# Kernel optimization log

Measured on AMD Instinct MI355X. Metric: run time of the kernel, lower is better.

Reference implementation:

```python
import jax, jax.numpy as jnp
import numpy as np
import math

B, C, N, M, K, TEMB, H = 16, 64, 4096, 257, 128, 256, 128
PI = math.pi

def _inv_sp(y):
    return math.log(math.expm1(y))

def setup_inputs():
    key = jax.random.key(0)
    ks = jax.random.split(key, 8)
    x_feat = jax.random.normal(ks[0], (B, C, N), jnp.float32)
    z = (jax.random.uniform(ks[1], (B, N), jnp.float32) * 2.0 - 1.0) * PI
    temb = jax.random.normal(ks[2], (B, TEMB), jnp.float32)
    kappa_pos_raw = jnp.full((K,), _inv_sp(0.3), jnp.float32)
    gabor_c = jnp.linspace(-1.0, 1.0, M).astype(jnp.float32)
    gabor_omega_raw = jnp.full((M,), _inv_sp(0.25), jnp.float32)
    wr = (jax.random.normal(ks[3], (C, M)) * 0.02).astype(jnp.float32)
    wi = (jax.random.normal(ks[4], (C, M)) * 0.02).astype(jnp.float32)
    bias = jnp.zeros((1, C, 1), jnp.float32)
    tproj_w = (jax.random.normal(ks[5], (C, TEMB)) * 0.02).astype(jnp.float32)
    tproj_b = jnp.zeros((C,), jnp.float32)
    mlp_w1 = (jax.random.normal(ks[6], (H, TEMB)) * 0.02).astype(jnp.float32)
    mlp_b1 = jnp.zeros((H,), jnp.float32)
    mlp_w2 = (jax.random.normal(ks[7], (1, H)) * 0.02).astype(jnp.float32)
    mlp_b2 = jnp.zeros((1,), jnp.float32)
    # tau0 = 0.15-quantile of |kappa_init| (matches ProgressiveFreqGate init)
    kpos0 = np.cumsum(np.log1p(np.exp(_inv_sp(0.3))) * np.ones(K, np.float64))
    kfull = np.concatenate([-kpos0[::-1], [0.0], kpos0])
    tau0 = jnp.float32(np.quantile(np.abs(kfull), 0.15))
    tau1_raw = jnp.float32(_inv_sp(0.5))
    alpha_raw = jnp.float32(_inv_sp(8.0))
    gate_low_raw = jnp.float32(4.0)
    gate_mid_raw = jnp.float32(-2.1972246)
    gate_high_raw = jnp.float32(-2.1972246)
    return dict(x_feat=x_feat, z=z, temb=temb, kappa_pos_raw=kappa_pos_raw,
                gabor_c=gabor_c, gabor_omega_raw=gabor_omega_raw, wr=wr, wi=wi,
                bias=bias, tproj_w=tproj_w, tproj_b=tproj_b, mlp_w1=mlp_w1,
                mlp_b1=mlp_b1, mlp_w2=mlp_w2, mlp_b2=mlp_b2, tau0=tau0,
                tau1_raw=tau1_raw, alpha_raw=alpha_raw, gate_low_raw=gate_low_raw,
                gate_mid_raw=gate_mid_raw, gate_high_raw=gate_high_raw)

def reference(x_feat, z, temb, kappa_pos_raw, gabor_c, gabor_omega_raw, wr, wi, bias,
              tproj_w, tproj_b, mlp_w1, mlp_b1, mlp_w2, mlp_b2,
              tau0, tau1_raw, alpha_raw, gate_low_raw, gate_mid_raw, gate_high_raw):
    sp = jax.nn.softplus
    # non-uniform learned frequencies: kappa = [-kpos[::-1], 0, kpos]
    kpos = jnp.cumsum(sp(kappa_pos_raw))                      # (K,)
    kappa = jnp.concatenate([-kpos[::-1], jnp.zeros((1,), kpos.dtype), kpos])  # (M,)
    k_abs = jax.lax.stop_gradient(jnp.abs(kappa))
    # band mask: quantile thresholds (detached), learnable low/mid/high gates
    th1 = jnp.quantile(k_abs, 0.4)
    th2 = jnp.quantile(k_abs, 0.8)
    g_low = jax.nn.sigmoid(gate_low_raw)
    g_mid = jax.nn.sigmoid(gate_mid_raw)
    g_high = jax.nn.sigmoid(gate_high_raw)
    band = jnp.where(k_abs <= th1, g_low, jnp.where(k_abs <= th2, g_mid, g_high))  # (M,)
    # progressive time-frequency gate: g = sigmoid(alpha*(tau(t) - |kappa|))
    hid = jax.nn.silu(temb @ mlp_w1.T + mlp_b1)               # (B,H)
    s_t = jnp.tanh(hid @ mlp_w2.T + mlp_b2)[:, 0]             # (B,)
    tau = tau0 + sp(tau1_raw) * s_t                           # (B,)
    alpha = sp(alpha_raw) + 1e-12
    g_tf = jax.nn.sigmoid(alpha * (tau[:, None] - k_abs[None, :]))  # (B,M)
    # time conditioning of features
    x = x_feat + (jax.nn.silu(temb) @ tproj_w.T + tproj_b)[:, :, None]  # (B,C,N)
    # non-uniform trig basis with Gabor window
    theta = z[:, :, None] * kappa[None, None, :]              # (B,N,M)
    omega = jnp.clip(sp(gabor_omega_raw), 1e-6)               # (M,)
    s_win = jnp.exp(-0.5 * ((z[:, :, None] / PI - gabor_c[None, None, :]) / omega) ** 2)
    cw = jnp.cos(theta) * s_win                               # (B,N,M)
    sw = jnp.sin(theta) * s_win                               # (B,N,M)
    n = x.shape[-1]
    # analysis (e^{-i theta}), normalized by N
    Xr = jnp.einsum('bcn,bnm->bcm', x, cw) / n                # (B,C,M)
    Xi = -jnp.einsum('bcn,bnm->bcm', x, sw) / n
    gate = band[None, None, :] * g_tf[:, None, :]             # (B,1,M)
    Xr = Xr * gate
    Xi = Xi * gate
    # separable complex spectral multiply
    Yr = Xr * wr[None] - Xi * wi[None]
    Yi = Xr * wi[None] + Xi * wr[None]
    # synthesis: Re(Y e^{+i theta}) with windowed basis
    out = jnp.einsum('bcm,bnm->bcn', Yr, cw) - jnp.einsum('bcm,bnm->bcn', Yi, sw)
    return out + bias
```

## Files before the change

kernel.cpp:

```cpp
#include <hip/hip_runtime.h>
#include <math.h>

#define NB 16
#define NCH 64
#define NPTS 4096
#define NM 257
#define NKF 128
#define NTEMB 256
#define NHID 128

#define MT 32
#define NMT 9
#define NCK 32
#define SMT 32
#define SNCK 64
#define NTILE 9

#define INV_PI 0.31830988618379067154f

typedef float v2f __attribute__((ext_vector_type(2)));

#define OFF_KAPPA 0
#define OFF_OMEGA 320
#define OFF_BAND  640
#define OFF_GATE  960
#define OFF_TCOND 5120
#define OFF_YR    6144
#define BMC       263168
#define OFF_YI    (OFF_YR + BMC)
#define OFF_PART  (OFF_YI + BMC)

__device__ __forceinline__ float sigf(float x){ return 1.0f/(1.0f+expf(-x)); }
__device__ __forceinline__ float softplusf(float x){ return (x>20.0f)? x : log1pf(expf(x)); }

__global__ void k_prep(const float* __restrict__ kraw, const float* __restrict__ gom,
                       const float* __restrict__ glow, const float* __restrict__ gmid,
                       const float* __restrict__ ghigh,
                       const float* __restrict__ temb,
                       const float* __restrict__ w1, const float* __restrict__ b1,
                       const float* __restrict__ w2, const float* __restrict__ b2,
                       const float* __restrict__ tprojw, const float* __restrict__ tprojb,
                       const float* __restrict__ tau0p, const float* __restrict__ tau1p,
                       const float* __restrict__ alphap,
                       float* __restrict__ ws){
  const int b = blockIdx.x;
  const int t = threadIdx.x;
  __shared__ float sp[NKF], kpos[NKF], th_s[2];
  __shared__ float te[NTEMB], ste[NTEMB], hid[NHID], red[64];
  __shared__ float tau_sh;

  if(t<NKF) sp[t] = softplusf(kraw[t]);
  {
    float v = temb[(size_t)b*NTEMB + t];
    te[t] = v;
    ste[t] = v * sigf(v);
  }
  __syncthreads();
  if(t==0){
    float acc = 0.0f;
    for(int k=0;k<NKF;k++){ acc += sp[k]; kpos[k]=acc; }
    th_s[0] = 0.6f*kpos[50]  + 0.4f*kpos[51];
    th_s[1] = 0.2f*kpos[101] + 0.8f*kpos[102];
  }
  if(t<NHID){
    float acc = b1[t];
    const float4* w4 = (const float4*)(w1 + (size_t)t*NTEMB);
    for(int k=0;k<NTEMB/4;k++){
      float4 wv = w4[k];
      acc = fmaf(te[4*k  ], wv.x, acc);
      acc = fmaf(te[4*k+1], wv.y, acc);
      acc = fmaf(te[4*k+2], wv.z, acc);
      acc = fmaf(te[4*k+3], wv.w, acc);
    }
    hid[t] = acc * sigf(acc);
  }
  __syncthreads();
  if(t<64) red[t] = hid[t]*w2[t] + hid[t+64]*w2[t+64];
  __syncthreads();
  if(t==0){
    float s = 0.0f;
    for(int i=0;i<64;i++) s += red[i];
    float st = tanhf(s + b2[0]);
    tau_sh = tau0p[0] + softplusf(tau1p[0])*st;
  }
  __syncthreads();
  const float th1 = th_s[0], th2 = th_s[1];
  const float alpha = softplusf(alphap[0]) + 1e-12f;
  const float tau = tau_sh;
  const float gl = sigf(glow[0]), gm = sigf(gmid[0]), gh = sigf(ghigh[0]);
  for(int m=t; m<NM; m+=256){
    float kap = (m<NKF) ? -kpos[NKF-1-m] : ((m==NKF) ? 0.0f : kpos[m-NKF-1]);
    float ka = fabsf(kap);
    float band = (ka<=th1) ? gl : ((ka<=th2) ? gm : gh);
    ws[OFF_GATE + b*NM + m] = band * sigf(alpha*(tau-ka));
    if(b==0){
      ws[OFF_KAPPA+m] = kap;
      ws[OFF_BAND +m] = band;
      ws[OFF_OMEGA+m] = fmaxf(softplusf(gom[m]), 1e-6f);
    }
  }
  if(t<NCH){
    float acc = tprojb[t];
    const float4* w4 = (const float4*)(tprojw + (size_t)t*NTEMB);
    for(int k=0;k<NTEMB/4;k++){
      float4 wv = w4[k];
      acc = fmaf(ste[4*k  ], wv.x, acc);
      acc = fmaf(ste[4*k+1], wv.y, acc);
      acc = fmaf(ste[4*k+2], wv.z, acc);
      acc = fmaf(ste[4*k+3], wv.w, acc);
    }
    ws[OFF_TCOND + b*NCH + t] = acc;
  }
}

__global__ __launch_bounds__(256, 8)
void k_analysis(const float* __restrict__ xf, const float* __restrict__ z,
                const float* __restrict__ gaborc,
                float* __restrict__ ws, int nsegLen){
  __shared__ float xs[NCH][36];
  __shared__ float cws[NCK][MT];
  __shared__ float sws[NCK][MT];
  __shared__ float zs[NCK];
  __shared__ float kap_s[MT], gc_s[MT], iom_s[MT];

  const int t = threadIdx.x;
  const int b = blockIdx.z, mt = blockIdx.x, ns = blockIdx.y;
  const int m0 = mt*MT;

  if(t<MT){
    int mg = min(m0+t, NM-1);
    kap_s[t] = ws[OFF_KAPPA+mg];
    gc_s[t]  = gaborc[mg];
    iom_s[t] = 1.0f/ws[OFF_OMEGA+mg];
  }

  const int cst = t>>2;
  const int j0  = (t&3)*4;
  const float tc = ws[OFF_TCOND + b*NCH + cst];

  const int mq = t&7;
  const int cg = t>>3;
  const int c0 = 2*cg;

  v2f ar0[2]={{0,0},{0,0}}, ai0[2]={{0,0},{0,0}};
  v2f ar1[2]={{0,0},{0,0}}, ai1[2]={{0,0},{0,0}};

  const int nbase0 = ns*nsegLen;
  const float* xrowBase = xf + ((size_t)b*NCH + cst)*NPTS;

  for(int nb = nbase0; nb < nbase0+nsegLen; nb += NCK){
    __syncthreads();
    if(t<NCK) zs[t] = z[(size_t)b*NPTS + nb + t];
    const float* xrow = xrowBase + nb;
    #pragma unroll
    for(int i=0;i<2;i++){
      float4 v = *(const float4*)(xrow + j0 + 16*i);
      v.x += tc; v.y += tc; v.z += tc; v.w += tc;
      *(float4*)&xs[cst][j0 + 16*i] = v;
    }
    __syncthreads();
    {
      const int m = t&31, nn = t>>5;
      const float kap = kap_s[m], gcv = gc_s[m], iom = iom_s[m];
      #pragma unroll
      for(int j=0;j<4;j++){
        int n = nn + 8*j;
        float zv = zs[n];
        float th = zv*kap;
        float sv = __sinf(th);
        float cv = __cosf(th);
        float e = fmaf(zv, INV_PI, -gcv)*iom;
        float w = __expf(-0.5f*e*e);
        cws[n][m] = cv*w;
        sws[n][m] = sv*w;
      }
    }
    __syncthreads();
    #pragma unroll 4
    for(int n=0;n<NCK;n++){
      float x0 = xs[c0  ][n];
      float x1 = xs[c0+1][n];
      float4 c4 = *(const float4*)&cws[n][mq*4];
      float4 s4 = *(const float4*)&sws[n][mq*4];
      v2f cA = {c4.x,c4.y}, cB = {c4.z,c4.w};
      v2f sA = {s4.x,s4.y}, sB = {s4.z,s4.w};
      v2f x0v = {x0,x0}, x1v = {x1,x1};
      ar0[0] = __builtin_elementwise_fma(x0v, cA, ar0[0]);
      ar0[1] = __builtin_elementwise_fma(x0v, cB, ar0[1]);
      ai0[0] = __builtin_elementwise_fma(x0v, sA, ai0[0]);
      ai0[1] = __builtin_elementwise_fma(x0v, sB, ai0[1]);
      ar1[0] = __builtin_elementwise_fma(x1v, cA, ar1[0]);
      ar1[1] = __builtin_elementwise_fma(x1v, cB, ar1[1]);
      ai1[0] = __builtin_elementwise_fma(x1v, sA, ai1[0]);
      ai1[1] = __builtin_elementwise_fma(x1v, sB, ai1[1]);
    }
  }
  const int NSg = gridDim.y;
  float* pr = ws + OFF_PART + (size_t)(ns*NB + b)*NM*NCH;
  float* pi = pr + (size_t)NSg*BMC;
  #pragma unroll
  for(int q=0;q<4;q++){
    int m = m0 + mq*4 + q;
    if(m < NM){
      pr[(size_t)m*NCH + c0  ] = ar0[q>>1][q&1];
      pr[(size_t)m*NCH + c0+1] = ar1[q>>1][q&1];
      pi[(size_t)m*NCH + c0  ] = ai0[q>>1][q&1];
      pi[(size_t)m*NCH + c0+1] = ai1[q>>1][q&1];
    }
  }
}

__global__ void k_reduce_mult(const float* __restrict__ wr, const float* __restrict__ wi,
                              float* __restrict__ ws, int NS){
  int idx = blockIdx.x*256 + threadIdx.x;
  if(idx >= BMC) return;
  int c = idx & 63;
  int m = (idx >> 6) % NM;
  int b = idx / (NM*NCH);
  const float* part = ws + OFF_PART;
  size_t ph = (size_t)NS*BMC;
  float sr=0.0f, si=0.0f;
  for(int s=0;s<NS;s++){
    size_t o = ((size_t)(s*NB + b)*NM + m)*NCH + c;
    sr += part[o];
    si += part[o+ph];
  }
  float g  = ws[OFF_GATE + b*NM + m] * (1.0f/(float)NPTS);
  float Xr =  g*sr;
  float Xi = -g*si;
  float wrv = wr[(size_t)c*NM+m], wiv = wi[(size_t)c*NM+m];
  ws[OFF_YR + idx] =   Xr*wrv - Xi*wiv;
  ws[OFF_YI + idx] = -(Xr*wiv + Xi*wrv);
}

__global__ __launch_bounds__(256, 4)
void k_synth(const float* __restrict__ z, const float* __restrict__ gaborc,
             const float* __restrict__ bias, const float* __restrict__ ws,
             float* __restrict__ out){
  __shared__ float yrs[SMT][64], yis[SMT][64];
  __shared__ float cws[SMT][68], sws[SMT][68];
  __shared__ float kapF[260], gcF[260], iomF[260];
  __shared__ float zs[SNCK];

  const int t = threadIdx.x;
  const int b = blockIdx.y;
  const int nb = blockIdx.x*SNCK;
  const int c0 = (t>>4)<<2;
  const int n0 = (t&15)<<2;

  for(int i=t; i<NM; i+=256){
    kapF[i] = ws[OFF_KAPPA+i];
    gcF[i]  = gaborc[i];
    iomF[i] = 1.0f/ws[OFF_OMEGA+i];
  }
  if(t<SNCK) zs[t] = z[(size_t)b*NPTS + nb + t];

  const float* yrBase = ws + OFF_YR + (size_t)b*NM*NCH;
  const float* yiBase = ws + OFF_YI + (size_t)b*NM*NCH;

  float4 pyr[2], pyi[2];
  #pragma unroll
  for(int e=0;e<2;e++){
    int s = t + e*256;
    pyr[e] = *(const float4*)(yrBase + (size_t)s*4);
    pyi[e] = *(const float4*)(yiBase + (size_t)s*4);
  }

  v2f acc[4][2] = {};

  for(int tile=0; tile<NTILE; tile++){
    const int mcb = tile*SMT;
    __syncthreads();
    #pragma unroll
    for(int e=0;e<2;e++){
      int s = t + e*256;
      int m = s>>4, cc = (s&15)<<2;
      *(float4*)&yrs[m][cc] = pyr[e];
      *(float4*)&yis[m][cc] = pyi[e];
    }
    {
      int n = t&63, mm = t>>6;
      float zv = zs[n], zp = zv*INV_PI;
      #pragma unroll
      for(int j=0;j<8;j++){
        int m = mm + 4*j;
        int mg = min(mcb+m, NM-1);
        float th = zv*kapF[mg];
        float sv = __sinf(th);
        float cv = __cosf(th);
        float e2 = (zp - gcF[mg])*iomF[mg];
        float w = __expf(-0.5f*e2*e2);
        cws[m][n] = cv*w;
        sws[m][n] = sv*w;
      }
    }
    __syncthreads();
    if(tile+1 < NTILE){
      const int mb2 = (tile+1)*SMT;
      #pragma unroll
      for(int e=0;e<2;e++){
        int s = t + e*256;
        int mglob = mb2 + (s>>4);
        if(mglob < NM){
          size_t o = (size_t)mb2*NCH + (size_t)s*4;
          pyr[e] = *(const float4*)(yrBase + o);
          pyi[e] = *(const float4*)(yiBase + o);
        } else {
          pyr[e] = make_float4(0,0,0,0);
          pyi[e] = make_float4(0,0,0,0);
        }
      }
    }
    #pragma unroll 4
    for(int m=0;m<SMT;m++){
      float4 yr4 = *(const float4*)&yrs[m][c0];
      float4 yi4 = *(const float4*)&yis[m][c0];
      v2f cA = *(const v2f*)&cws[m][n0];
      v2f cB = *(const v2f*)&cws[m][n0+2];
      v2f sA = *(const v2f*)&sws[m][n0];
      v2f sB = *(const v2f*)&sws[m][n0+2];
      float yrv[4]={yr4.x,yr4.y,yr4.z,yr4.w};
      float yiv[4]={yi4.x,yi4.y,yi4.z,yi4.w};
      #pragma unroll
      for(int a=0;a<4;a++){
        v2f yr = {yrv[a],yrv[a]};
        v2f yi = {yiv[a],yiv[a]};
        acc[a][0] = __builtin_elementwise_fma(yr, cA, acc[a][0]);
        acc[a][0] = __builtin_elementwise_fma(yi, sA, acc[a][0]);
        acc[a][1] = __builtin_elementwise_fma(yr, cB, acc[a][1]);
        acc[a][1] = __builtin_elementwise_fma(yi, sB, acc[a][1]);
      }
    }
  }
  #pragma unroll
  for(int a=0;a<4;a++){
    int c = c0 + a;
    float bv = bias[c];
    float4 v;
    v.x = acc[a][0][0]+bv; v.y = acc[a][0][1]+bv;
    v.z = acc[a][1][0]+bv; v.w = acc[a][1][1]+bv;
    *(float4*)(out + ((size_t)b*NCH + c)*NPTS + nb + n0) = v;
  }
}

extern "C" void kernel_launch(void* const* d_in, const int* in_sizes, int n_in,
                              void* d_out, int out_size, void* d_ws, size_t ws_size,
                              hipStream_t stream){
  const float* x_feat = (const float*)d_in[0];
  const float* z      = (const float*)d_in[1];
  const float* temb   = (const float*)d_in[2];
  const float* kraw   = (const float*)d_in[3];
  const float* gaborc = (const float*)d_in[4];
  const float* gom    = (const float*)d_in[5];
  const float* wr     = (const float*)d_in[6];
  const float* wi     = (const float*)d_in[7];
  const float* bias   = (const float*)d_in[8];
  const float* tprojw = (const float*)d_in[9];
  const float* tprojb = (const float*)d_in[10];
  const float* w1     = (const float*)d_in[11];
  const float* b1     = (const float*)d_in[12];
  const float* w2     = (const float*)d_in[13];
  const float* b2     = (const float*)d_in[14];
  const float* tau0   = (const float*)d_in[15];
  const float* tau1   = (const float*)d_in[16];
  const float* alphar = (const float*)d_in[17];
  const float* glow   = (const float*)d_in[18];
  const float* gmid   = (const float*)d_in[19];
  const float* ghigh  = (const float*)d_in[20];
  float* out = (float*)d_out;
  float* ws  = (float*)d_ws;

  int NS = 8;
  while(NS > 1 && ws_size < (size_t)(OFF_PART + 2*(size_t)NS*BMC)*sizeof(float)) NS >>= 1;

  k_prep      <<<NB, 256, 0, stream>>>(kraw, gom, glow, gmid, ghigh, temb,
                                       w1, b1, w2, b2, tprojw, tprojb,
                                       tau0, tau1, alphar, ws);
  k_analysis  <<<dim3(NMT, NS, NB), 256, 0, stream>>>(x_feat, z, gaborc, ws, NPTS/NS);
  k_reduce_mult<<<(BMC+255)/256, 256, 0, stream>>>(wr, wi, ws, NS);
  k_synth     <<<dim3(NPTS/SNCK, NB), 256, 0, stream>>>(z, gaborc, bias, ws, out);
}
```

Before: 271.6 us.

## Move analysis GEMM onto bf16 MFMA with split hi/lo precision compensation

Rewrites the analysis kernel to compute the windowed trig basis straight into registers, then accumulate with 16x16x32 bf16 MFMA instructions in place of scalar packed FMAs. Accuracy is kept by splitting both operands into high and low bf16 parts and issuing three MFMAs per product. The basis moves out of shared memory, the m-tile doubles to 64, and the N-split count rises to 16 for more parallelism. The cost is a larger partial-sum buffer for the reduce kernel, extra conversion work per chunk, and a possible small loss of accuracy.

```diff
diff --git a/kernel.cpp b/kernel.cpp
--- a/kernel.cpp
+++ b/kernel.cpp
@@ -9,9 +9,9 @@
 #define NTEMB 256
 #define NHID 128
 
-#define MT 32
-#define NMT 9
-#define NCK 32
+#define AMT 64
+#define ANMT 5
+#define ANCK 32
 #define SMT 32
 #define SNCK 64
 #define NTILE 9
@@ -19,6 +19,9 @@
 #define INV_PI 0.31830988618379067154f
 
 typedef float v2f __attribute__((ext_vector_type(2)));
+typedef short bf16x8 __attribute__((ext_vector_type(8)));
+typedef float f32x4 __attribute__((ext_vector_type(4)));
+typedef unsigned short u16;
 
 #define OFF_KAPPA 0
 #define OFF_OMEGA 320
@@ -32,6 +35,12 @@
 
 __device__ __forceinline__ float sigf(float x){ return 1.0f/(1.0f+expf(-x)); }
 __device__ __forceinline__ float softplusf(float x){ return (x>20.0f)? x : log1pf(expf(x)); }
+__device__ __forceinline__ u16 f2bf(float f){
+  unsigned u = __float_as_uint(f);
+  u += 0x7fffu + ((u>>16)&1u);
+  return (u16)(u>>16);
+}
+__device__ __forceinline__ float bf2f(u16 h){ return __uint_as_float(((unsigned)h)<<16); }
 
 __global__ void k_prep(const float* __restrict__ kraw, const float* __restrict__ gom,
                        const float* __restrict__ glow, const float* __restrict__ gmid,
@@ -113,99 +122,104 @@
   }
 }
 
-__global__ __launch_bounds__(256, 8)
+__global__ __launch_bounds__(256, 4)
 void k_analysis(const float* __restrict__ xf, const float* __restrict__ z,
                 const float* __restrict__ gaborc,
                 float* __restrict__ ws, int nsegLen){
-  __shared__ float xs[NCH][36];
-  __shared__ float cws[NCK][MT];
-  __shared__ float sws[NCK][MT];
-  __shared__ float zs[NCK];
-  __shared__ float kap_s[MT], gc_s[MT], iom_s[MT];
+  __shared__ u16 xhi[NCH][40], xlo[NCH][40];
+  __shared__ float zs[ANCK];
+  __shared__ float kapA[AMT], gcA[AMT], iomA[AMT];
 
   const int t = threadIdx.x;
   const int b = blockIdx.z, mt = blockIdx.x, ns = blockIdx.y;
-  const int m0 = mt*MT;
-
-  if(t<MT){
+  const int m0 = mt*AMT;
+
+  if(t<AMT){
     int mg = min(m0+t, NM-1);
-    kap_s[t] = ws[OFF_KAPPA+mg];
-    gc_s[t]  = gaborc[mg];
-    iom_s[t] = 1.0f/ws[OFF_OMEGA+mg];
-  }
+    kapA[t] = ws[OFF_KAPPA+mg];
+    gcA[t]  = gaborc[mg];
+    iomA[t] = 1.0f/ws[OFF_OMEGA+mg];
+  }
+  __syncthreads();
+
+  const int w  = t>>6;
+  const int l  = t&63;
+  const int lc = l&15;
+  const int kb = (l>>4)*8;
+  const float mkap = kapA[w*16+lc], mgc = gcA[w*16+lc], miom = iomA[w*16+lc];
 
   const int cst = t>>2;
-  const int j0  = (t&3)*4;
+  const int j0  = (t&3)*8;
   const float tc = ws[OFF_TCOND + b*NCH + cst];
 
-  const int mq = t&7;
-  const int cg = t>>3;
-  const int c0 = 2*cg;
-
-  v2f ar0[2]={{0,0},{0,0}}, ai0[2]={{0,0},{0,0}};
-  v2f ar1[2]={{0,0},{0,0}}, ai1[2]={{0,0},{0,0}};
+  f32x4 accR[4] = {{0,0,0,0},{0,0,0,0},{0,0,0,0},{0,0,0,0}};
+  f32x4 accI[4] = {{0,0,0,0},{0,0,0,0},{0,0,0,0},{0,0,0,0}};
 
   const int nbase0 = ns*nsegLen;
-  const float* xrowBase = xf + ((size_t)b*NCH + cst)*NPTS;
-
-  for(int nb = nbase0; nb < nbase0+nsegLen; nb += NCK){
+  const float* xrow = xf + ((size_t)b*NCH + cst)*NPTS;
+
+  for(int nb2 = nbase0; nb2 < nbase0+nsegLen; nb2 += ANCK){
     __syncthreads();
-    if(t<NCK) zs[t] = z[(size_t)b*NPTS + nb + t];
-    const float* xrow = xrowBase + nb;
+    if(t<ANCK) zs[t] = z[(size_t)b*NPTS + nb2 + t];
+    {
+      float4 v0 = *(const float4*)(xrow + nb2 + j0);
+      float4 v1 = *(const float4*)(xrow + nb2 + j0 + 4);
+      float vals[8] = {v0.x+tc, v0.y+tc, v0.z+tc, v0.w+tc,
+                       v1.x+tc, v1.y+tc, v1.z+tc, v1.w+tc};
+      bf16x8 ph, pl;
+      #pragma unroll
+      for(int i=0;i<8;i++){
+        u16 h = f2bf(vals[i]);
+        ph[i] = (short)h;
+        pl[i] = (short)f2bf(vals[i] - bf2f(h));
+      }
+      *(bf16x8*)&xhi[cst][j0] = ph;
+      *(bf16x8*)&xlo[cst][j0] = pl;
+    }
+    __syncthreads();
+
+    bf16x8 cwh, cwl, swh, swl;
     #pragma unroll
-    for(int i=0;i<2;i++){
-      float4 v = *(const float4*)(xrow + j0 + 16*i);
-      v.x += tc; v.y += tc; v.z += tc; v.w += tc;
-      *(float4*)&xs[cst][j0 + 16*i] = v;
-    }
-    __syncthreads();
-    {
-      const int m = t&31, nn = t>>5;
-      const float kap = kap_s[m], gcv = gc_s[m], iom = iom_s[m];
-      #pragma unroll
-      for(int j=0;j<4;j++){
-        int n = nn + 8*j;
-        float zv = zs[n];
-        float th = zv*kap;
-        float sv = __sinf(th);
-        float cv = __cosf(th);
-        float e = fmaf(zv, INV_PI, -gcv)*iom;
-        float w = __expf(-0.5f*e*e);
-        cws[n][m] = cv*w;
-        sws[n][m] = sv*w;
-      }
-    }
-    __syncthreads();
-    #pragma unroll 4
-    for(int n=0;n<NCK;n++){
-      float x0 = xs[c0  ][n];
-      float x1 = xs[c0+1][n];
-      float4 c4 = *(const float4*)&cws[n][mq*4];
-      float4 s4 = *(const float4*)&sws[n][mq*4];
-      v2f cA = {c4.x,c4.y}, cB = {c4.z,c4.w};
-      v2f sA = {s4.x,s4.y}, sB = {s4.z,s4.w};
-      v2f x0v = {x0,x0}, x1v = {x1,x1};
-      ar0[0] = __builtin_elementwise_fma(x0v, cA, ar0[0]);
-      ar0[1] = __builtin_elementwise_fma(x0v, cB, ar0[1]);
-      ai0[0] = __builtin_elementwise_fma(x0v, sA, ai0[0]);
-      ai0[1] = __builtin_elementwise_fma(x0v, sB, ai0[1]);
-      ar1[0] = __builtin_elementwise_fma(x1v, cA, ar1[0]);
-      ar1[1] = __builtin_elementwise_fma(x1v, cB, ar1[1]);
-      ai1[0] = __builtin_elementwise_fma(x1v, sA, ai1[0]);
-      ai1[1] = __builtin_elementwise_fma(x1v, sB, ai1[1]);
-    }
-  }
+    for(int j=0;j<8;j++){
+      float zv = zs[kb + j];
+      float th = zv*mkap;
+      float sv = __sinf(th);
+      float cv = __cosf(th);
+      float e  = fmaf(zv, INV_PI, -mgc)*miom;
+      float wv = __expf(-0.5f*e*e);
+      float cwf = cv*wv, swf = sv*wv;
+      u16 ch = f2bf(cwf);
+      cwh[j] = (short)ch; cwl[j] = (short)f2bf(cwf - bf2f(ch));
+      u16 sh = f2bf(swf);
+      swh[j] = (short)sh; swl[j] = (short)f2bf(swf - bf2f(sh));
+    }
+
+    #pragma unroll
+    for(int cs=0; cs<4; cs++){
+      bf16x8 bh = *(const bf16x8*)&xhi[cs*16 + lc][kb];
+      bf16x8 bl = *(const bf16x8*)&xlo[cs*16 + lc][kb];
+      accR[cs] = __builtin_amdgcn_mfma_f32_16x16x32_bf16(cwh, bh, accR[cs], 0,0,0);
+      accR[cs] = __builtin_amdgcn_mfma_f32_16x16x32_bf16(cwl, bh, accR[cs], 0,0,0);
+      accR[cs] = __builtin_amdgcn_mfma_f32_16x16x32_bf16(cwh, bl, accR[cs], 0,0,0);
+      accI[cs] = __builtin_amdgcn_mfma_f32_16x16x32_bf16(swh, bh, accI[cs], 0,0,0);
+      accI[cs] = __builtin_amdgcn_mfma_f32_16x16x32_bf16(swl, bh, accI[cs], 0,0,0);
+      accI[cs] = __builtin_amdgcn_mfma_f32_16x16x32_bf16(swh, bl, accI[cs], 0,0,0);
+    }
+  }
+
   const int NSg = gridDim.y;
   float* pr = ws + OFF_PART + (size_t)(ns*NB + b)*NM*NCH;
   float* pi = pr + (size_t)NSg*BMC;
   #pragma unroll
-  for(int q=0;q<4;q++){
-    int m = m0 + mq*4 + q;
-    if(m < NM){
-      pr[(size_t)m*NCH + c0  ] = ar0[q>>1][q&1];
-      pr[(size_t)m*NCH + c0+1] = ar1[q>>1][q&1];
-      pi[(size_t)m*NCH + c0  ] = ai0[q>>1][q&1];
-      pi[(size_t)m*NCH + c0+1] = ai1[q>>1][q&1];
+  for(int cs=0; cs<4; cs++){
+    #pragma unroll
+    for(int r=0;r<4;r++){
+      int m_out = m0 + w*16 + (l>>4)*4 + r;
+      int c_out = cs*16 + lc;
+      if(m_out < NM){
+        pr[(size_t)m_out*NCH + c_out] = accR[cs][r];
+        pi[(size_t)m_out*NCH + c_out] = accI[cs][r];
+      }
     }
   }
 }
@@ -370,13 +384,13 @@
   float* out = (float*)d_out;
   float* ws  = (float*)d_ws;
 
-  int NS = 8;
+  int NS = 16;
   while(NS > 1 && ws_size < (size_t)(OFF_PART + 2*(size_t)NS*BMC)*sizeof(float)) NS >>= 1;
 
   k_prep      <<<NB, 256, 0, stream>>>(kraw, gom, glow, gmid, ghigh, temb,
                                        w1, b1, w2, b2, tprojw, tprojb,
                                        tau0, tau1, alphar, ws);
-  k_analysis  <<<dim3(NMT, NS, NB), 256, 0, stream>>>(x_feat, z, gaborc, ws, NPTS/NS);
+  k_analysis  <<<dim3(ANMT, NS, NB), 256, 0, stream>>>(x_feat, z, gaborc, ws, NPTS/NS);
   k_reduce_mult<<<(BMC+255)/256, 256, 0, stream>>>(wr, wi, ws, NS);
   k_synth     <<<dim3(NPTS/SNCK, NB), 256, 0, stream>>>(z, gaborc, bias, ws, out);
 }
```

Result: faster. 223.3 us (-17.8%).
